# Performance work log

Hardware: AMD Instinct MI355X
Metric: run time of the kernel (lower is better)

Reference implementation:

```python
import jax, jax.numpy as jnp
import numpy as np

N, T, B = 883, 12, 64
DIN, DOUT, CHEB_K, DE = 2, 64, 2, 10


def setup_inputs() -> dict:
    key = jax.random.key(0)
    ks = jax.random.split(key, 12)
    x = jax.random.normal(ks[0], (B, T, N, DIN), dtype=jnp.float32)
    adj = jax.random.uniform(ks[1], (N, N), dtype=jnp.float32) / N  # roughly row-stochastic
    node_embeddings = jax.random.normal(ks[2], (N, DE), dtype=jnp.float32)
    s = 0.05
    DI = DIN + DOUT
    # forward-direction cell pools (AGCRN-style)
    Wg_f = jax.random.normal(ks[3], (DE, CHEB_K, DI, 2 * DOUT), dtype=jnp.float32) * s
    bg_f = jax.random.normal(ks[4], (DE, 2 * DOUT), dtype=jnp.float32) * s
    Wc_f = jax.random.normal(ks[5], (DE, CHEB_K, DI, DOUT), dtype=jnp.float32) * s
    bc_f = jax.random.normal(ks[6], (DE, DOUT), dtype=jnp.float32) * s
    # backward-direction cell pools
    Wg_b = jax.random.normal(ks[7], (DE, CHEB_K, DI, 2 * DOUT), dtype=jnp.float32) * s
    bg_b = jax.random.normal(ks[8], (DE, 2 * DOUT), dtype=jnp.float32) * s
    Wc_b = jax.random.normal(ks[9], (DE, CHEB_K, DI, DOUT), dtype=jnp.float32) * s
    bc_b = jax.random.normal(ks[10], (DE, DOUT), dtype=jnp.float32) * s
    return {"x": x, "adj": adj, "node_embeddings": node_embeddings,
            "Wg_f": Wg_f, "bg_f": bg_f, "Wc_f": Wc_f, "bc_f": bc_f,
            "Wg_b": Wg_b, "bg_b": bg_b, "Wc_b": Wc_b, "bc_b": bc_b}


def _cheb_supports(adj, E):
    # adaptive adjacency from node embeddings (AGCRN) combined with given adj
    A = jax.nn.softmax(jax.nn.relu(E @ E.T), axis=1)
    S = A + adj
    polys = [jnp.eye(N, dtype=S.dtype), S]
    for _ in range(2, CHEB_K):
        polys.append(2.0 * S @ polys[-1] - polys[-2])
    return jnp.stack(polys[:CHEB_K])  # [K,N,N]


def _run_direction(x_seq, adj, E, Wg, bg, Wc, bc):
    supports = _cheb_supports(adj, E)                 # [K,N,N]
    Wg_n = jnp.einsum('nd,dkio->nkio', E, Wg)         # [N,K,DI,2*DOUT]
    bg_n = E @ bg                                     # [N,2*DOUT]
    Wc_n = jnp.einsum('nd,dkio->nkio', E, Wc)
    bc_n = E @ bc

    def gconv(inp, Wn, bn):
        xg = jnp.einsum('knm,bmi->bkni', supports, inp)
        return jnp.einsum('bkni,nkio->bno', xg, Wn) + bn

    def step(h, xt):
        inp = jnp.concatenate([xt, h], axis=-1)       # [B,N,DI]
        zr = jax.nn.sigmoid(gconv(inp, Wg_n, bg_n))
        z, r = jnp.split(zr, 2, axis=-1)
        inp2 = jnp.concatenate([xt, r * h], axis=-1)
        hc = jnp.tanh(gconv(inp2, Wc_n, bc_n))
        h_new = z * h + (1.0 - z) * hc
        return h_new, h_new

    h0 = jnp.zeros((x_seq.shape[0], N, DOUT), dtype=x_seq.dtype)
    _, hs = jax.lax.scan(step, h0, jnp.swapaxes(x_seq, 0, 1))  # [T,B,N,DOUT]
    return jnp.swapaxes(hs, 0, 1)                              # [B,T,N,DOUT]


def reference(x, adj, node_embeddings, Wg_f, bg_f, Wc_f, bc_f, Wg_b, bg_b, Wc_b, bc_b):
    out1 = _run_direction(x, adj, node_embeddings, Wg_f, bg_f, Wc_f, bc_f)
    out2 = _run_direction(jnp.flip(x, axis=1), adj, node_embeddings, Wg_b, bg_b, Wc_b, bc_b)
    # BiSTFGRN assigns out2 without re-flipping; stay faithful.
    return jnp.concatenate([out1, out2], axis=-1)  # [B,T,N,2*DOUT]
```

## Files before the change

### kernel.cpp

```cpp
#include <hip/hip_runtime.h>
#include <math.h>

#define N_NODES 883
#define KPAD 896
#define T_STEPS 12
#define DE 10
#define KI 132
#define NCOLS 8192
#define XCOLS 1536
#define WSTR 160
#define ASTR 168
#define GOSTR (128 * WSTR)
#define COSTR (64 * WSTR)
#define BK 64

typedef _Float16 f16;
typedef __attribute__((ext_vector_type(2))) _Float16 f16x2;
typedef __attribute__((ext_vector_type(4))) _Float16 f16x4;
typedef __attribute__((ext_vector_type(8))) _Float16 f16x8;
typedef __attribute__((ext_vector_type(4))) float f32x4;

__device__ inline void gload16(const void* g, void* l) {
    __builtin_amdgcn_global_load_lds(
        (const __attribute__((address_space(1))) unsigned int*)g,
        (__attribute__((address_space(3))) unsigned int*)l, 16, 0, 0);
}

__global__ __launch_bounds__(256) void k_computeS(const float* __restrict__ E,
                                                  const float* __restrict__ adj,
                                                  f16* __restrict__ Sh) {
    int n = blockIdx.x;
    int tid = threadIdx.x;
    __shared__ float l[N_NODES];
    __shared__ float red[8];
    float En[DE];
#pragma unroll
    for (int d = 0; d < DE; ++d) En[d] = E[n * DE + d];

    float lmax = -1e30f;
    for (int m = tid; m < N_NODES; m += 256) {
        float dot = 0.f;
#pragma unroll
        for (int d = 0; d < DE; ++d) dot += En[d] * E[m * DE + d];
        dot = fmaxf(dot, 0.f);
        l[m] = dot;
        lmax = fmaxf(lmax, dot);
    }
    int wave = tid >> 6, lane = tid & 63;
    for (int off = 32; off > 0; off >>= 1) lmax = fmaxf(lmax, __shfl_down(lmax, off));
    if (lane == 0) red[wave] = lmax;
    __syncthreads();
    float gmax = fmaxf(fmaxf(red[0], red[1]), fmaxf(red[2], red[3]));
    __syncthreads();

    float lsum = 0.f;
    for (int m = tid; m < N_NODES; m += 256) {
        float e = expf(l[m] - gmax);
        l[m] = e;
        lsum += e;
    }
    for (int off = 32; off > 0; off >>= 1) lsum += __shfl_down(lsum, off);
    if (lane == 0) red[wave] = lsum;
    __syncthreads();
    float inv = 1.0f / (red[0] + red[1] + red[2] + red[3]);
    for (int m = tid; m < N_NODES; m += 256) {
        Sh[(size_t)n * KPAD + m] = (f16)(l[m] * inv + adj[(size_t)n * N_NODES + m]);
    }
}

__global__ void k_buildXT(const float* __restrict__ x, f16* __restrict__ XTt) {
    int idx = blockIdx.x * blockDim.x + threadIdx.x;
    if (idx >= XCOLS * N_NODES) return;
    int m = idx % N_NODES;
    int c = idx / N_NODES;
    int t = c >> 7;
    int b = (c >> 1) & 63;
    int i = c & 1;
    XTt[(size_t)c * KPAD + m] = (f16)x[(((size_t)b * T_STEPS + t) * N_NODES + m) * 2 + i];
}

__global__ void k_reorgW(const float* __restrict__ Wg_f, const float* __restrict__ Wg_b,
                         const float* __restrict__ Wc_f, const float* __restrict__ Wc_b,
                         const float* __restrict__ bg_f, const float* __restrict__ bg_b,
                         const float* __restrict__ bc_f, const float* __restrict__ bc_b,
                         float* __restrict__ Wg_r, float* __restrict__ Wc_r) {
    const int GTOT = 2 * DE * GOSTR;
    const int CTOT = 2 * DE * COSTR;
    int idx = blockIdx.x * blockDim.x + threadIdx.x;
    if (idx < GTOT) {
        int k = idx % WSTR;
        int o = (idx / WSTR) & 127;
        int d = (idx / GOSTR) % DE;
        int dir = idx / (DE * GOSTR);
        float v = 0.f;
        if (k < KI) {
            const float* W = dir ? Wg_b : Wg_f;
            int kc = k / 66, i = k % 66;
            v = W[(((size_t)d * 2 + kc) * 66 + i) * 128 + o];
        } else if (k == KI) {
            v = (dir ? bg_b : bg_f)[d * 128 + o];
        }
        Wg_r[idx] = v;
    } else if (idx < GTOT + CTOT) {
        int j = idx - GTOT;
        int k = j % WSTR;
        int o = (j / WSTR) & 63;
        int d = (j / COSTR) % DE;
        int dir = j / (DE * COSTR);
        float v = 0.f;
        if (k < KI) {
            const float* W = dir ? Wc_b : Wc_f;
            int kc = k / 66, i = k % 66;
            v = W[(((size_t)d * 2 + kc) * 66 + i) * 64 + o];
        } else if (k == KI) {
            v = (dir ? bc_b : bc_f)[d * 64 + o];
        }
        Wc_r[j] = v;
    }
}

__global__ __launch_bounds__(256) void k_buildW2(
    const float* __restrict__ E,
    const float* __restrict__ Wg_r, const float* __restrict__ Wc_r,
    f16* __restrict__ WgT, f16* __restrict__ WcT) {
    int grp = blockIdx.x, dir = blockIdx.y, z = blockIdx.z;
    int n0 = grp * 16;
    int tid = threadIdx.x;
    __shared__ float Es[16][DE];
    if (tid < 16 * DE) {
        int nn = tid / DE, d = tid % DE;
        int n = n0 + nn;
        Es[nn][d] = (n < N_NODES) ? E[n * DE + d] : 0.f;
    }
    __syncthreads();

    bool gate = z < 4;
    const float* src = gate ? (Wg_r + (size_t)dir * DE * GOSTR)
                            : (Wc_r + (size_t)dir * DE * COSTR);
    f16* dst = gate ? WgT : WcT;
    int ostr = gate ? GOSTR : COSTR;
    int slot0 = gate ? z * 1280 : (z - 4) * 1280;

#pragma unroll
    for (int it = 0; it < 5; ++it) {
        int f = (slot0 + it * 256 + tid) * 4;
        float4 v[DE];
#pragma unroll
        for (int d = 0; d < DE; ++d)
            v[d] = *(const float4*)&src[(size_t)d * ostr + f];
#pragma unroll
        for (int nn = 0; nn < 16; ++nn) {
            int n = n0 + nn;
            if (n >= N_NODES) break;
            float a0 = 0.f, a1 = 0.f, a2 = 0.f, a3 = 0.f;
#pragma unroll
            for (int d = 0; d < DE; ++d) {
                float e = Es[nn][d];
                a0 += e * v[d].x; a1 += e * v[d].y;
                a2 += e * v[d].z; a3 += e * v[d].w;
            }
            f16x4 r = {(f16)a0, (f16)a1, (f16)a2, (f16)a3};
            *(f16x4*)&dst[(size_t)(dir * N_NODES + n) * ostr + f] = r;
        }
    }
}

__global__ __launch_bounds__(256) void k_transpose(const f16* __restrict__ V,
                                                   f16* __restrict__ VT) {
    __shared__ f16 tile[64][66];
    int c0 = blockIdx.x * 64;
    int n0 = blockIdx.y * 64;
    int tid = threadIdx.x;
#pragma unroll
    for (int it = 0; it < 2; ++it) {
        int chunk = tid + it * 256;
        int r = chunk >> 3, g = chunk & 7;
        int n = n0 + r;
        f16 tmp[8];
        if (n < N_NODES) {
            f16x8 v = *(const f16x8*)&V[(size_t)n * NCOLS + c0 + g * 8];
#pragma unroll
            for (int j = 0; j < 8; ++j) tmp[j] = v[j];
        } else {
#pragma unroll
            for (int j = 0; j < 8; ++j) tmp[j] = (f16)0.f;
        }
#pragma unroll
        for (int j = 0; j < 8; ++j) tile[g * 8 + j][r] = tmp[j];
    }
    __syncthreads();
#pragma unroll
    for (int it = 0; it < 2; ++it) {
        int chunk = tid + it * 256;
        int cc = chunk >> 3, m = chunk & 7;
        f16x8 v;
#pragma unroll
        for (int j = 0; j < 8; ++j) v[j] = tile[cc][m * 8 + j];
        *(f16x8*)&VT[(size_t)(c0 + cc) * KPAD + n0 + m * 8] = v;
    }
}

__global__ __launch_bounds__(256) void k_gemm_f16(const f16* __restrict__ A,
                                                  const f16* __restrict__ Bt,
                                                  f16* __restrict__ C, int NC) {
    __shared__ f16 Als[128 * BK];
    __shared__ f16 Bls[64 * BK];
    int tid = threadIdx.x;
    int w = tid >> 6, l = tid & 63;
    int wr = w >> 1, wc = w & 1;
    int row0 = blockIdx.y * 128;
    int col0 = blockIdx.x * 64;
    int lr = l & 15, lg = l >> 4;

    int sr = l >> 3;
    int gslot = (l & 7) ^ sr;
    const f16* ga = A + (size_t)(row0 + w * 32 + sr) * KPAD + gslot * 8;
    const f16* gb = Bt + (size_t)(col0 + w * 16 + sr) * KPAD + gslot * 8;

    f32x4 acc[4][2];
#pragma unroll
    for (int m = 0; m < 4; ++m)
#pragma unroll
        for (int n = 0; n < 2; ++n) acc[m][n] = (f32x4)(0.f);

    for (int kt = 0; kt < KPAD / BK; ++kt) {
        int k0 = kt * BK;
#pragma unroll
        for (int c = 0; c < 4; ++c)
            gload16(ga + (size_t)(c * 8) * KPAD + k0, &Als[(w * 32 + c * 8) * BK]);
#pragma unroll
        for (int c = 0; c < 2; ++c)
            gload16(gb + (size_t)(c * 8) * KPAD + k0, &Bls[(w * 16 + c * 8) * BK]);
        __syncthreads();
#pragma unroll
        for (int ks = 0; ks < 2; ++ks) {
            int slot = (ks * 4 + lg) ^ (lr & 7);
            f16x8 af[4], bf[2];
#pragma unroll
            for (int m = 0; m < 4; ++m)
                af[m] = *(const f16x8*)&Als[(wr * 64 + m * 16 + lr) * BK + slot * 8];
#pragma unroll
            for (int n = 0; n < 2; ++n)
                bf[n] = *(const f16x8*)&Bls[(wc * 32 + n * 16 + lr) * BK + slot * 8];
#pragma unroll
            for (int m = 0; m < 4; ++m)
#pragma unroll
                for (int n = 0; n < 2; ++n)
                    acc[m][n] = __builtin_amdgcn_mfma_f32_16x16x32_f16(af[m], bf[n], acc[m][n], 0, 0, 0);
        }
        __syncthreads();
    }

#pragma unroll
    for (int m = 0; m < 4; ++m) {
        int gr0 = row0 + wr * 64 + m * 16 + lg * 4;
#pragma unroll
        for (int n = 0; n < 2; ++n) {
            int gc = col0 + wc * 32 + n * 16 + lr;
            f32x4 v = acc[m][n];
#pragma unroll
            for (int q = 0; q < 4; ++q) {
                int r = gr0 + q;
                if (r < N_NODES) C[(size_t)r * NC + gc] = (f16)v[q];
            }
        }
    }
}

__global__ __launch_bounds__(256) void k_apply_gate(
    const float* __restrict__ x, const f16* __restrict__ Hh,
    const f16* __restrict__ SXh, const f16* __restrict__ SHh,
    const f16* __restrict__ WgT,
    f16* __restrict__ Zh, f16* __restrict__ RHh, int t, int first) {
    int n = blockIdx.x, dir = blockIdx.y;
    int tid = threadIdx.x;
    int tt = dir ? (T_STEPS - 1 - t) : t;
    __shared__ f16 inpA[64 * ASTR];

    const f16* hhrow = Hh + (size_t)n * NCOLS + dir * 4096;
    const f16* shrow = SHh + (size_t)n * NCOLS + dir * 4096;

#pragma unroll
    for (int it = 0; it < 8; ++it) {
        int i2 = tid + it * 256;
        int b = i2 >> 5, jp = i2 & 31;
        *(unsigned*)&inpA[b * ASTR + 2 + 2 * jp] = *(const unsigned*)&hhrow[b * 64 + 2 * jp];
        *(unsigned*)&inpA[b * ASTR + 68 + 2 * jp] =
            first ? 0u : *(const unsigned*)&shrow[b * 64 + 2 * jp];
    }
    if (tid < 128) {
        int b = tid >> 1, i = tid & 1;
        inpA[b * ASTR + i] = (f16)x[(((size_t)b * T_STEPS + tt) * N_NODES + n) * 2 + i];
        inpA[b * ASTR + 66 + i] = SXh[(size_t)n * XCOLS + tt * 128 + b * 2 + i];
    }
    for (int idx = tid; idx < 64 * 14; idx += 256) {
        int b = idx / 14, p = idx % 14;
        *(unsigned*)&inpA[b * ASTR + 132 + 2 * p] = (p == 0) ? 0x00003C00u : 0u;
    }
    __syncthreads();

    int w = tid >> 6, l = tid & 63;
    int lr = l & 15, lg = l >> 4;
    int o0 = w * 32;
    const f16* wbase = WgT + (size_t)(dir * N_NODES + n) * GOSTR;

    f32x4 acc[4][2];
#pragma unroll
    for (int m = 0; m < 4; ++m)
#pragma unroll
        for (int j = 0; j < 2; ++j) acc[m][j] = (f32x4)(0.f);

#pragma unroll
    for (int kt = 0; kt < 5; ++kt) {
        int k0 = kt * 32 + lg * 8;
        f16x8 af[4], bf[2];
#pragma unroll
        for (int m = 0; m < 4; ++m)
            af[m] = *(const f16x8*)&inpA[(m * 16 + lr) * ASTR + k0];
#pragma unroll
        for (int j = 0; j < 2; ++j)
            bf[j] = *(const f16x8*)&wbase[(size_t)(o0 + j * 16 + lr) * WSTR + k0];
#pragma unroll
        for (int m = 0; m < 4; ++m)
#pragma unroll
            for (int j = 0; j < 2; ++j)
                acc[m][j] = __builtin_amdgcn_mfma_f32_16x16x32_f16(af[m], bf[j], acc[m][j], 0, 0, 0);
    }

    f16* zrow = Zh + (size_t)(dir * N_NODES + n) * 4096;
    f16* rhrow = RHh + (size_t)n * NCOLS + dir * 4096;
#pragma unroll
    for (int j = 0; j < 2; ++j) {
        int o = o0 + j * 16 + lr;
        if (o < 64) {
#pragma unroll
            for (int m = 0; m < 4; ++m) {
                int b0 = m * 16 + lg * 4;
                f32x4 v = acc[m][j];
#pragma unroll
                for (int q = 0; q < 4; ++q)
                    zrow[(b0 + q) * 64 + o] = (f16)(1.f / (1.f + expf(-v[q])));
            }
        } else {
            int jj = o - 64;
#pragma unroll
            for (int m = 0; m < 4; ++m) {
                int b0 = m * 16 + lg * 4;
                f32x4 v = acc[m][j];
#pragma unroll
                for (int q = 0; q < 4; ++q) {
                    float r = 1.f / (1.f + expf(-v[q]));
                    rhrow[(b0 + q) * 64 + jj] =
                        (f16)(r * (float)hhrow[(b0 + q) * 64 + jj]);
                }
            }
        }
    }
}

__global__ __launch_bounds__(256) void k_apply_cand(
    const float* __restrict__ x, const f16* __restrict__ SXh,
    const f16* __restrict__ SRHh, const f16* __restrict__ RHh,
    const f16* __restrict__ WcT, const f16* __restrict__ Zh,
    f16* __restrict__ Hh, float* __restrict__ out, int t, int last) {
    int n = blockIdx.x, dir = blockIdx.y;
    int tid = threadIdx.x;
    int tt = dir ? (T_STEPS - 1 - t) : t;
    __shared__ f16 inpA[64 * ASTR];

    const f16* rhrow = RHh + (size_t)n * NCOLS + dir * 4096;
    const f16* srhrow = SRHh + (size_t)n * NCOLS + dir * 4096;

#pragma unroll
    for (int it = 0; it < 8; ++it) {
        int i2 = tid + it * 256;
        int b = i2 >> 5, jp = i2 & 31;
        *(unsigned*)&inpA[b * ASTR + 2 + 2 * jp] = *(const unsigned*)&rhrow[b * 64 + 2 * jp];
        *(unsigned*)&inpA[b * ASTR + 68 + 2 * jp] = *(const unsigned*)&srhrow[b * 64 + 2 * jp];
    }
    if (tid < 128) {
        int b = tid >> 1, i = tid & 1;
        inpA[b * ASTR + i] = (f16)x[(((size_t)b * T_STEPS + tt) * N_NODES + n) * 2 + i];
        inpA[b * ASTR + 66 + i] = SXh[(size_t)n * XCOLS + tt * 128 + b * 2 + i];
    }
    for (int idx = tid; idx < 64 * 14; idx += 256) {
        int b = idx / 14, p = idx % 14;
        *(unsigned*)&inpA[b * ASTR + 132 + 2 * p] = (p == 0) ? 0x00003C00u : 0u;
    }
    __syncthreads();

    int w = tid >> 6, l = tid & 63;
    int lr = l & 15, lg = l >> 4;
    const f16* wbase = WcT + (size_t)(dir * N_NODES + n) * COSTR;

    f32x4 acc[4];
#pragma unroll
    for (int j = 0; j < 4; ++j) acc[j] = (f32x4)(0.f);

#pragma unroll
    for (int kt = 0; kt < 5; ++kt) {
        int k0 = kt * 32 + lg * 8;
        f16x8 af = *(const f16x8*)&inpA[(w * 16 + lr) * ASTR + k0];
        f16x8 bf[4];
#pragma unroll
        for (int j = 0; j < 4; ++j)
            bf[j] = *(const f16x8*)&wbase[(size_t)(j * 16 + lr) * WSTR + k0];
#pragma unroll
        for (int j = 0; j < 4; ++j)
            acc[j] = __builtin_amdgcn_mfma_f32_16x16x32_f16(af, bf[j], acc[j], 0, 0, 0);
    }

    const f16* zrow = Zh + (size_t)(dir * N_NODES + n) * 4096;
    f16* hhrow = Hh + (size_t)n * NCOLS + dir * 4096;
#pragma unroll
    for (int j = 0; j < 4; ++j) {
        int o = j * 16 + lr;
        f32x4 v = acc[j];
#pragma unroll
        for (int q = 0; q < 4; ++q) {
            int b = w * 16 + lg * 4 + q;
            float hc = tanhf(v[q]);
            float zv = (float)zrow[b * 64 + o];
            float hp = (float)hhrow[b * 64 + o];
            float hn = zv * hp + (1.f - zv) * hc;
            if (!last) hhrow[b * 64 + o] = (f16)hn;
            out[(((size_t)b * T_STEPS + t) * N_NODES + n) * 128 + dir * 64 + o] = hn;
        }
    }
}

extern "C" void kernel_launch(void* const* d_in, const int* in_sizes, int n_in,
                              void* d_out, int out_size, void* d_ws, size_t ws_size,
                              hipStream_t stream) {
    const float* x    = (const float*)d_in[0];
    const float* adj  = (const float*)d_in[1];
    const float* E    = (const float*)d_in[2];
    const float* Wg_f = (const float*)d_in[3];
    const float* bg_f = (const float*)d_in[4];
    const float* Wc_f = (const float*)d_in[5];
    const float* bc_f = (const float*)d_in[6];
    const float* Wg_b = (const float*)d_in[7];
    const float* bg_b = (const float*)d_in[8];
    const float* Wc_b = (const float*)d_in[9];
    const float* bc_b = (const float*)d_in[10];
    float* out = (float*)d_out;

    size_t off = 0;
    auto alloc = [&](size_t bytes) {
        void* p = (char*)d_ws + off;
        off += (bytes + 255) & ~(size_t)255;
        return p;
    };
    f16*   Sh   = (f16*)alloc((size_t)KPAD * KPAD * 2);
    f16*   XTt  = (f16*)alloc((size_t)XCOLS * KPAD * 2);
    f16*   SXh  = (f16*)alloc((size_t)N_NODES * XCOLS * 2);
    f16*   Hh   = (f16*)alloc((size_t)N_NODES * NCOLS * 2);
    f16*   SHh  = (f16*)alloc((size_t)N_NODES * NCOLS * 2);
    f16*   RHh  = (f16*)alloc((size_t)N_NODES * NCOLS * 2);
    f16*   Zh   = (f16*)alloc((size_t)N_NODES * NCOLS * 2);
    f16*   HBt  = (f16*)alloc((size_t)NCOLS * KPAD * 2);
    f16*   RHBt = (f16*)alloc((size_t)NCOLS * KPAD * 2);
    f16*   WgT  = (f16*)alloc((size_t)2 * N_NODES * GOSTR * 2);
    f16*   WcT  = (f16*)alloc((size_t)2 * N_NODES * COSTR * 2);
    float* Wg_r = (float*)RHBt;
    float* Wc_r = Wg_r + (size_t)2 * DE * GOSTR;

    hipMemsetAsync(Sh, 0, (size_t)KPAD * KPAD * 2, stream);
    hipMemsetAsync(XTt, 0, (size_t)XCOLS * KPAD * 2, stream);
    hipMemsetAsync(Hh, 0, (size_t)N_NODES * NCOLS * 2, stream);

    k_computeS<<<N_NODES, 256, 0, stream>>>(E, adj, Sh);
    {
        int total = XCOLS * N_NODES;
        k_buildXT<<<(total + 255) / 256, 256, 0, stream>>>(x, XTt);
    }
    {
        int total = 2 * DE * (GOSTR + COSTR);
        k_reorgW<<<(total + 255) / 256, 256, 0, stream>>>(Wg_f, Wg_b, Wc_f, Wc_b,
                                                          bg_f, bg_b, bc_f, bc_b,
                                                          Wg_r, Wc_r);
    }
    k_buildW2<<<dim3(56, 2, 6), 256, 0, stream>>>(E, Wg_r, Wc_r, WgT, WcT);
    k_gemm_f16<<<dim3(XCOLS / 64, 7), 256, 0, stream>>>(Sh, XTt, SXh, XCOLS);

    dim3 gnode(N_NODES, 2);
    dim3 gmain(NCOLS / 64, 7);
    dim3 gtr(NCOLS / 64, KPAD / 64);
    for (int t = 0; t < T_STEPS; ++t) {
        if (t > 0)
            k_gemm_f16<<<gmain, 256, 0, stream>>>(Sh, HBt, SHh, NCOLS);
        k_apply_gate<<<gnode, 256, 0, stream>>>(x, Hh, SXh, SHh, WgT,
                                                Zh, RHh, t, t == 0 ? 1 : 0);
        k_transpose<<<gtr, 256, 0, stream>>>(RHh, RHBt);
        k_gemm_f16<<<gmain, 256, 0, stream>>>(Sh, RHBt, SHh, NCOLS);
        k_apply_cand<<<gnode, 256, 0, stream>>>(x, SXh, SHh, RHh, WcT,
                                                Zh, Hh, out, t,
                                                t == T_STEPS - 1 ? 1 : 0);
        if (t < T_STEPS - 1)
            k_transpose<<<gtr, 256, 0, stream>>>(Hh, HBt);
    }
}
```

Measured before the change: 1.499 ms.

## Remove per-step transposes by loading row-major B tiles directly in GEMM

The GEMM now reads the hidden-state operand in its native node-major layout and transposes it into LDS on the fly, so the two transpose kernels per timestep are dropped. The memsets are removed too: the computeS kernel now writes its own zero padding, and the first step treats the previous hidden state as zero. This saves two launches and the extra global traffic each step. The cost is that B is now loaded through registers with scalar LDS stores, which may cause bank conflicts, instead of async global-to-LDS loads.

```diff
diff --git a/kernel.cpp b/kernel.cpp
--- a/kernel.cpp
+++ b/kernel.cpp
@@ -13,6 +13,7 @@
 #define GOSTR (128 * WSTR)
 #define COSTR (64 * WSTR)
 #define BK 64
+#define BTS 72
 
 typedef _Float16 f16;
 typedef __attribute__((ext_vector_type(2))) _Float16 f16x2;
@@ -63,20 +64,22 @@
     if (lane == 0) red[wave] = lsum;
     __syncthreads();
     float inv = 1.0f / (red[0] + red[1] + red[2] + red[3]);
-    for (int m = tid; m < N_NODES; m += 256) {
-        Sh[(size_t)n * KPAD + m] = (f16)(l[m] * inv + adj[(size_t)n * N_NODES + m]);
-    }
-}
-
-__global__ void k_buildXT(const float* __restrict__ x, f16* __restrict__ XTt) {
+    for (int m = tid; m < KPAD; m += 256) {
+        f16 val = (f16)0.f;
+        if (m < N_NODES) val = (f16)(l[m] * inv + adj[(size_t)n * N_NODES + m]);
+        Sh[(size_t)n * KPAD + m] = val;
+    }
+}
+
+__global__ void k_buildXT(const float* __restrict__ x, f16* __restrict__ XTr) {
     int idx = blockIdx.x * blockDim.x + threadIdx.x;
-    if (idx >= XCOLS * N_NODES) return;
-    int m = idx % N_NODES;
-    int c = idx / N_NODES;
+    if (idx >= N_NODES * XCOLS) return;
+    int c = idx % XCOLS;
+    int m = idx / XCOLS;
     int t = c >> 7;
     int b = (c >> 1) & 63;
     int i = c & 1;
-    XTt[(size_t)c * KPAD + m] = (f16)x[(((size_t)b * T_STEPS + t) * N_NODES + m) * 2 + i];
+    XTr[(size_t)m * XCOLS + c] = (f16)x[(((size_t)b * T_STEPS + t) * N_NODES + m) * 2 + i];
 }
 
 __global__ void k_reorgW(const float* __restrict__ Wg_f, const float* __restrict__ Wg_b,
@@ -165,46 +168,11 @@
     }
 }
 
-__global__ __launch_bounds__(256) void k_transpose(const f16* __restrict__ V,
-                                                   f16* __restrict__ VT) {
-    __shared__ f16 tile[64][66];
-    int c0 = blockIdx.x * 64;
-    int n0 = blockIdx.y * 64;
-    int tid = threadIdx.x;
-#pragma unroll
-    for (int it = 0; it < 2; ++it) {
-        int chunk = tid + it * 256;
-        int r = chunk >> 3, g = chunk & 7;
-        int n = n0 + r;
-        f16 tmp[8];
-        if (n < N_NODES) {
-            f16x8 v = *(const f16x8*)&V[(size_t)n * NCOLS + c0 + g * 8];
-#pragma unroll
-            for (int j = 0; j < 8; ++j) tmp[j] = v[j];
-        } else {
-#pragma unroll
-            for (int j = 0; j < 8; ++j) tmp[j] = (f16)0.f;
-        }
-#pragma unroll
-        for (int j = 0; j < 8; ++j) tile[g * 8 + j][r] = tmp[j];
-    }
-    __syncthreads();
-#pragma unroll
-    for (int it = 0; it < 2; ++it) {
-        int chunk = tid + it * 256;
-        int cc = chunk >> 3, m = chunk & 7;
-        f16x8 v;
-#pragma unroll
-        for (int j = 0; j < 8; ++j) v[j] = tile[cc][m * 8 + j];
-        *(f16x8*)&VT[(size_t)(c0 + cc) * KPAD + n0 + m * 8] = v;
-    }
-}
-
-__global__ __launch_bounds__(256) void k_gemm_f16(const f16* __restrict__ A,
-                                                  const f16* __restrict__ Bt,
-                                                  f16* __restrict__ C, int NC) {
+__global__ __launch_bounds__(256) void k_gemm_rm(const f16* __restrict__ A,
+                                                 const f16* __restrict__ V,
+                                                 f16* __restrict__ C, int NC) {
     __shared__ f16 Als[128 * BK];
-    __shared__ f16 Bls[64 * BK];
+    __shared__ f16 Bt_ls[64 * BTS];
     int tid = threadIdx.x;
     int w = tid >> 6, l = tid & 63;
     int wr = w >> 1, wc = w & 1;
@@ -215,7 +183,9 @@
     int sr = l >> 3;
     int gslot = (l & 7) ^ sr;
     const f16* ga = A + (size_t)(row0 + w * 32 + sr) * KPAD + gslot * 8;
-    const f16* gb = Bt + (size_t)(col0 + w * 16 + sr) * KPAD + gslot * 8;
+
+    int bk_row = tid >> 3;
+    int bc0 = (tid & 7) * 8;
 
     f32x4 acc[4][2];
 #pragma unroll
@@ -229,8 +199,20 @@
         for (int c = 0; c < 4; ++c)
             gload16(ga + (size_t)(c * 8) * KPAD + k0, &Als[(w * 32 + c * 8) * BK]);
 #pragma unroll
-        for (int c = 0; c < 2; ++c)
-            gload16(gb + (size_t)(c * 8) * KPAD + k0, &Bls[(w * 16 + c * 8) * BK]);
+        for (int pass = 0; pass < 2; ++pass) {
+            int kk = bk_row + pass * 32;
+            int kglob = k0 + kk;
+            f16x8 v;
+            if (kglob < N_NODES)
+                v = *(const f16x8*)&V[(size_t)kglob * NC + col0 + bc0];
+            else {
+#pragma unroll
+                for (int e = 0; e < 8; ++e) v[e] = (f16)0.f;
+            }
+#pragma unroll
+            for (int e = 0; e < 8; ++e)
+                Bt_ls[(bc0 + e) * BTS + kk] = v[e];
+        }
         __syncthreads();
 #pragma unroll
         for (int ks = 0; ks < 2; ++ks) {
@@ -241,7 +223,7 @@
                 af[m] = *(const f16x8*)&Als[(wr * 64 + m * 16 + lr) * BK + slot * 8];
 #pragma unroll
             for (int n = 0; n < 2; ++n)
-                bf[n] = *(const f16x8*)&Bls[(wc * 32 + n * 16 + lr) * BK + slot * 8];
+                bf[n] = *(const f16x8*)&Bt_ls[(wc * 32 + n * 16 + lr) * BTS + (ks * 4 + lg) * 8];
 #pragma unroll
             for (int m = 0; m < 4; ++m)
 #pragma unroll
@@ -284,7 +266,8 @@
     for (int it = 0; it < 8; ++it) {
         int i2 = tid + it * 256;
         int b = i2 >> 5, jp = i2 & 31;
-        *(unsigned*)&inpA[b * ASTR + 2 + 2 * jp] = *(const unsigned*)&hhrow[b * 64 + 2 * jp];
+        *(unsigned*)&inpA[b * ASTR + 2 + 2 * jp] =
+            first ? 0u : *(const unsigned*)&hhrow[b * 64 + 2 * jp];
         *(unsigned*)&inpA[b * ASTR + 68 + 2 * jp] =
             first ? 0u : *(const unsigned*)&shrow[b * 64 + 2 * jp];
     }
@@ -350,8 +333,8 @@
 #pragma unroll
                 for (int q = 0; q < 4; ++q) {
                     float r = 1.f / (1.f + expf(-v[q]));
-                    rhrow[(b0 + q) * 64 + jj] =
-                        (f16)(r * (float)hhrow[(b0 + q) * 64 + jj]);
+                    float hp = first ? 0.f : (float)hhrow[(b0 + q) * 64 + jj];
+                    rhrow[(b0 + q) * 64 + jj] = (f16)(r * hp);
                 }
             }
         }
@@ -362,7 +345,7 @@
     const float* __restrict__ x, const f16* __restrict__ SXh,
     const f16* __restrict__ SRHh, const f16* __restrict__ RHh,
     const f16* __restrict__ WcT, const f16* __restrict__ Zh,
-    f16* __restrict__ Hh, float* __restrict__ out, int t, int last) {
+    f16* __restrict__ Hh, float* __restrict__ out, int t, int first, int last) {
     int n = blockIdx.x, dir = blockIdx.y;
     int tid = threadIdx.x;
     int tt = dir ? (T_STEPS - 1 - t) : t;
@@ -421,7 +404,7 @@
             int b = w * 16 + lg * 4 + q;
             float hc = tanhf(v[q]);
             float zv = (float)zrow[b * 64 + o];
-            float hp = (float)hhrow[b * 64 + o];
+            float hp = first ? 0.f : (float)hhrow[b * 64 + o];
             float hn = zv * hp + (1.f - zv) * hc;
             if (!last) hhrow[b * 64 + o] = (f16)hn;
             out[(((size_t)b * T_STEPS + t) * N_NODES + n) * 128 + dir * 64 + o] = hn;
@@ -452,27 +435,21 @@
         return p;
     };
     f16*   Sh   = (f16*)alloc((size_t)KPAD * KPAD * 2);
-    f16*   XTt  = (f16*)alloc((size_t)XCOLS * KPAD * 2);
+    f16*   XTr  = (f16*)alloc((size_t)KPAD * XCOLS * 2);
     f16*   SXh  = (f16*)alloc((size_t)N_NODES * XCOLS * 2);
     f16*   Hh   = (f16*)alloc((size_t)N_NODES * NCOLS * 2);
     f16*   SHh  = (f16*)alloc((size_t)N_NODES * NCOLS * 2);
     f16*   RHh  = (f16*)alloc((size_t)N_NODES * NCOLS * 2);
     f16*   Zh   = (f16*)alloc((size_t)N_NODES * NCOLS * 2);
-    f16*   HBt  = (f16*)alloc((size_t)NCOLS * KPAD * 2);
-    f16*   RHBt = (f16*)alloc((size_t)NCOLS * KPAD * 2);
     f16*   WgT  = (f16*)alloc((size_t)2 * N_NODES * GOSTR * 2);
     f16*   WcT  = (f16*)alloc((size_t)2 * N_NODES * COSTR * 2);
-    float* Wg_r = (float*)RHBt;
-    float* Wc_r = Wg_r + (size_t)2 * DE * GOSTR;
-
-    hipMemsetAsync(Sh, 0, (size_t)KPAD * KPAD * 2, stream);
-    hipMemsetAsync(XTt, 0, (size_t)XCOLS * KPAD * 2, stream);
-    hipMemsetAsync(Hh, 0, (size_t)N_NODES * NCOLS * 2, stream);
+    float* Wg_r = (float*)alloc((size_t)2 * DE * GOSTR * 4);
+    float* Wc_r = (float*)alloc((size_t)2 * DE * COSTR * 4);
 
     k_computeS<<<N_NODES, 256, 0, stream>>>(E, adj, Sh);
     {
-        int total = XCOLS * N_NODES;
-        k_buildXT<<<(total + 255) / 256, 256, 0, stream>>>(x, XTt);
+        int total = N_NODES * XCOLS;
+        k_buildXT<<<(total + 255) / 256, 256, 0, stream>>>(x, XTr);
     }
     {
         int total = 2 * DE * (GOSTR + COSTR);
@@ -481,22 +458,19 @@
                                                           Wg_r, Wc_r);
     }
     k_buildW2<<<dim3(56, 2, 6), 256, 0, stream>>>(E, Wg_r, Wc_r, WgT, WcT);
-    k_gemm_f16<<<dim3(XCOLS / 64, 7), 256, 0, stream>>>(Sh, XTt, SXh, XCOLS);
+    k_gemm_rm<<<dim3(XCOLS / 64, 7), 256, 0, stream>>>(Sh, XTr, SXh, XCOLS);
 
     dim3 gnode(N_NODES, 2);
     dim3 gmain(NCOLS / 64, 7);
-    dim3 gtr(NCOLS / 64, KPAD / 64);
     for (int t = 0; t < T_STEPS; ++t) {
         if (t > 0)
-            k_gemm_f16<<<gmain, 256, 0, stream>>>(Sh, HBt, SHh, NCOLS);
+            k_gemm_rm<<<gmain, 256, 0, stream>>>(Sh, Hh, SHh, NCOLS);
         k_apply_gate<<<gnode, 256, 0, stream>>>(x, Hh, SXh, SHh, WgT,
                                                 Zh, RHh, t, t == 0 ? 1 : 0);
-        k_transpose<<<gtr, 256, 0, stream>>>(RHh, RHBt);
-        k_gemm_f16<<<gmain, 256, 0, stream>>>(Sh, RHBt, SHh, NCOLS);
+        k_gemm_rm<<<gmain, 256, 0, stream>>>(Sh, RHh, SHh, NCOLS);
         k_apply_cand<<<gnode, 256, 0, stream>>>(x, SXh, SHh, RHh, WcT,
                                                 Zh, Hh, out, t,
+                                                t == 0 ? 1 : 0,
                                                 t == T_STEPS - 1 ? 1 : 0);
-        if (t < T_STEPS - 1)
-            k_transpose<<<gtr, 256, 0, stream>>>(Hh, HBt);
-    }
-}
+    }
+}
```

Result: slower. 1.923 ms (+28.3%).
